# Performance work log

Hardware: AMD Instinct MI355X
Metric: run time of the kernel (lower is better)

## Reference

```python
import jax, jax.numpy as jnp
import numpy as np
import math

D_MODEL = 1024
NUM_HEADS = 16
HEAD_DIM = D_MODEL // NUM_HEADS


def _xavier(key, out_f, in_f):
    limit = math.sqrt(6.0 / (in_f + out_f))
    return jax.random.uniform(key, (out_f, in_f), jnp.float32, -limit, limit)


def ternarize(w):
    # abs-mean threshold -> {-1, 0, +1}
    abs_mean = jnp.mean(jnp.abs(w))
    return jnp.where(jnp.abs(w) > abs_mean, jnp.sign(w), jnp.zeros_like(w))


def setup_inputs() -> dict:
    key = jax.random.key(0)
    kq, kk, kv, kwq, kwk, kwv, kwo = jax.random.split(key, 7)
    B, S = 2, 2048
    return {
        "query": jax.random.normal(kq, (B, S, D_MODEL), jnp.float32),
        "key": jax.random.normal(kk, (B, S, D_MODEL), jnp.float32),
        "value": jax.random.normal(kv, (B, S, D_MODEL), jnp.float32),
        "w_q": _xavier(kwq, D_MODEL, D_MODEL),
        "w_k": _xavier(kwk, D_MODEL, D_MODEL),
        "w_v": _xavier(kwv, D_MODEL, D_MODEL),
        "w_o": _xavier(kwo, D_MODEL, D_MODEL),
    }


def reference(query, key, value, w_q, w_k, w_v, w_o):
    B, S, _ = query.shape
    # ternary projections (F.linear: x @ W.T)
    q = query @ ternarize(w_q).T
    k = key @ ternarize(w_k).T
    v = value @ ternarize(w_v).T
    # [B, H, S, Dh]
    q = q.reshape(B, S, NUM_HEADS, HEAD_DIM).transpose(0, 2, 1, 3)
    k = k.reshape(B, -1, NUM_HEADS, HEAD_DIM).transpose(0, 2, 1, 3)
    v = v.reshape(B, -1, NUM_HEADS, HEAD_DIM).transpose(0, 2, 1, 3)
    scores = jnp.einsum("bhqd,bhkd->bhqk", q, k) / math.sqrt(HEAD_DIM)
    probs = jax.nn.softmax(scores, axis=-1)
    out = jnp.einsum("bhqk,bhkd->bhqd", probs, v)
    out = out.transpose(0, 2, 1, 3).reshape(B, S, D_MODEL)
    return out @ ternarize(w_o).T
```

## Files before the change

### kernel.cpp

```cpp
#include <hip/hip_runtime.h>
#include <cstdint>
#include <cstddef>

typedef __bf16 bfloat;
typedef __bf16 bf16x8 __attribute__((ext_vector_type(8)));
typedef __bf16 bf16x4 __attribute__((ext_vector_type(4)));
typedef float  f32x4  __attribute__((ext_vector_type(4)));

static constexpr int D  = 1024;
static constexpr int S  = 2048;
static constexpr int B  = 2;
static constexpr int H  = 16;
static constexpr int DH = 64;
static constexpr int M  = B * S;
static constexpr int WMAT_N = 1024 * 1024;

#define MFMA_BF16(a, b, c) __builtin_amdgcn_mfma_f32_16x16x32_bf16((a), (b), (c), 0, 0, 0)

__device__ __forceinline__ void gl_lds16(const void* g, void* l) {
  __builtin_amdgcn_global_load_lds(
      (const __attribute__((address_space(1))) void*)g,
      (__attribute__((address_space(3))) void*)l, 16, 0, 0);
}

__global__ void prep_kernel(const float* __restrict__ w0, const float* __restrict__ w1,
                            const float* __restrict__ w2, const float* __restrict__ w3,
                            const float* __restrict__ qx, const float* __restrict__ kx,
                            const float* __restrict__ vx, bfloat* __restrict__ qhi,
                            bfloat* __restrict__ qlo, bfloat* __restrict__ khi,
                            bfloat* __restrict__ klo, bfloat* __restrict__ vhi,
                            double* __restrict__ sums) {
  const int y = blockIdx.y;
  if (y < 4) {
    const float* w = (y == 0) ? w0 : (y == 1) ? w1 : (y == 2) ? w2 : w3;
    const float4* w4 = (const float4*)w;
    double s = 0.0;
    for (int i = blockIdx.x * blockDim.x + threadIdx.x; i < (WMAT_N / 4);
         i += gridDim.x * blockDim.x) {
      float4 v = w4[i];
      s += (double)fabsf(v.x) + (double)fabsf(v.y) + (double)fabsf(v.z) + (double)fabsf(v.w);
    }
    for (int off = 1; off < 64; off <<= 1) s += __shfl_xor(s, off, 64);
    __shared__ double ps[4];
    if ((threadIdx.x & 63) == 0) ps[threadIdx.x >> 6] = s;
    __syncthreads();
    if (threadIdx.x == 0) atomicAdd(&sums[y], ps[0] + ps[1] + ps[2] + ps[3]);
  } else {
    const int z = y - 4;
    const float* x = (z == 0) ? qx : (z == 1) ? kx : vx;
    bfloat* hi = (z == 0) ? qhi : (z == 1) ? khi : vhi;
    bfloat* lo = (z == 0) ? qlo : (z == 1) ? klo : nullptr;
    const int n8 = M * D / 8;
    const float4* x4 = (const float4*)x;
    for (int i = blockIdx.x * blockDim.x + threadIdx.x; i < n8;
         i += gridDim.x * blockDim.x) {
      float4 a = x4[2 * i], b = x4[2 * i + 1];
      float f[8] = {a.x, a.y, a.z, a.w, b.x, b.y, b.z, b.w};
      bf16x8 h;
#pragma unroll
      for (int j = 0; j < 8; j++) h[j] = (bfloat)f[j];
      *(bf16x8*)&hi[(size_t)i * 8] = h;
      if (z < 2) {
        bf16x8 l;
#pragma unroll
        for (int j = 0; j < 8; j++) l[j] = (bfloat)(f[j] - (float)h[j]);
        *(bf16x8*)&lo[(size_t)i * 8] = l;
      }
    }
  }
}

__global__ void tern_kernel(const float* __restrict__ w0, const float* __restrict__ w1,
                            const float* __restrict__ w2, const float* __restrict__ w3,
                            bfloat* __restrict__ o0, bfloat* __restrict__ o1,
                            bfloat* __restrict__ o2, bfloat* __restrict__ o3,
                            const double* __restrict__ sums) {
  int z = blockIdx.y;
  const float* w = (z == 0) ? w0 : (z == 1) ? w1 : (z == 2) ? w2 : w3;
  bfloat* o = (z == 0) ? o0 : (z == 1) ? o1 : (z == 2) ? o2 : o3;
  double thr = sums[z] * (1.0 / (double)WMAT_N);
  const float4* w4 = (const float4*)w;
  for (int i = blockIdx.x * blockDim.x + threadIdx.x; i < (WMAT_N / 4);
       i += gridDim.x * blockDim.x) {
    float4 v = w4[i];
    bf16x4 r;
    r[0] = (bfloat)(((double)fabsf(v.x) > thr) ? (v.x > 0.f ? 1.f : -1.f) : 0.f);
    r[1] = (bfloat)(((double)fabsf(v.y) > thr) ? (v.y > 0.f ? 1.f : -1.f) : 0.f);
    r[2] = (bfloat)(((double)fabsf(v.z) > thr) ? (v.z > 0.f ? 1.f : -1.f) : 0.f);
    r[3] = (bfloat)(((double)fabsf(v.w) > thr) ? (v.w > 0.f ? 1.f : -1.f) : 0.f);
    *(bf16x4*)&o[(size_t)i * 4] = r;
  }
}

__global__ __launch_bounds__(256) void qkv_gemm(
    const bfloat* __restrict__ xqh, const bfloat* __restrict__ xql,
    const bfloat* __restrict__ xkh, const bfloat* __restrict__ xkl,
    const bfloat* __restrict__ xvh, const bfloat* __restrict__ wqt,
    const bfloat* __restrict__ wkt, const bfloat* __restrict__ wvt,
    bfloat* __restrict__ qmh, bfloat* __restrict__ qml,
    bfloat* __restrict__ kmh, bfloat* __restrict__ kml, bfloat* __restrict__ vtr) {
  constexpr int K = D;
  constexpr int N = D;
  __shared__ __align__(16) bfloat As0[128 * 64];
  __shared__ __align__(16) bfloat As1[128 * 64];
  __shared__ __align__(16) bfloat Ws[128 * 64];

  const int z = blockIdx.z;
  const bfloat *A0, *A1 = nullptr, *Wm;
  bfloat *Oh = nullptr, *Ol = nullptr;
  float scale = 1.f;
  bool split;
  if (z == 0) {
    A0 = xqh; A1 = xql; Wm = wqt; Oh = qmh; Ol = qml;
    scale = 0.18033688f;
    split = true;
  } else if (z == 1) {
    A0 = xkh; A1 = xkl; Wm = wkt; Oh = kmh; Ol = kml; split = true;
  } else {
    A0 = xvh; Wm = wvt; split = false;
  }

  const int t = threadIdx.x;
  const int w = t >> 6, lane = t & 63;
  const int quad = lane >> 4, l16 = lane & 15;
  const int wm = w >> 1, wn = w & 1;
  const int m0 = blockIdx.y * 128, n0 = blockIdx.x * 128;

  f32x4 acc[4][4] = {};

  const int srr = lane >> 3;
  const int spc = lane & 7;

  for (int kk = 0; kk < K; kk += 64) {
#pragma unroll
    for (int g = 0; g < 4; g++) {
      int row = w * 32 + g * 8 + srr;
      int cl = spc ^ (row & 7);
      int lo = (w * 32 + g * 8) * 64;
      gl_lds16(A0 + (size_t)(m0 + row) * K + kk + cl * 8, As0 + lo);
      if (split) gl_lds16(A1 + (size_t)(m0 + row) * K + kk + cl * 8, As1 + lo);
      gl_lds16(Wm + (size_t)(n0 + row) * K + kk + cl * 8, Ws + lo);
    }
    __syncthreads();

#pragma unroll
    for (int kidx = 0; kidx < 2; kidx++) {
      bf16x8 bfrag[4], afrag[4];
#pragma unroll
      for (int nt = 0; nt < 4; nt++) {
        int r = wn * 64 + nt * 16 + l16;
        bfrag[nt] = *(const bf16x8*)&Ws[r * 64 + (((kidx * 4 + quad) ^ (r & 7)) * 8)];
      }
#pragma unroll
      for (int mt = 0; mt < 4; mt++) {
        int r = wm * 64 + mt * 16 + l16;
        afrag[mt] = *(const bf16x8*)&As0[r * 64 + (((kidx * 4 + quad) ^ (r & 7)) * 8)];
      }
#pragma unroll
      for (int mt = 0; mt < 4; mt++)
#pragma unroll
        for (int nt = 0; nt < 4; nt++)
          acc[mt][nt] = MFMA_BF16(afrag[mt], bfrag[nt], acc[mt][nt]);
      if (split) {
#pragma unroll
        for (int mt = 0; mt < 4; mt++) {
          int r = wm * 64 + mt * 16 + l16;
          afrag[mt] = *(const bf16x8*)&As1[r * 64 + (((kidx * 4 + quad) ^ (r & 7)) * 8)];
        }
#pragma unroll
        for (int mt = 0; mt < 4; mt++)
#pragma unroll
          for (int nt = 0; nt < 4; nt++)
            acc[mt][nt] = MFMA_BF16(afrag[mt], bfrag[nt], acc[mt][nt]);
      }
    }
    __syncthreads();
  }

#pragma unroll
  for (int mt = 0; mt < 4; mt++) {
#pragma unroll
    for (int nt = 0; nt < 4; nt++) {
      const int row = m0 + wm * 64 + mt * 16 + quad * 4;
      const int col = n0 + wn * 64 + nt * 16 + l16;
      if (split) {
#pragma unroll
        for (int rg = 0; rg < 4; rg++) {
          float vv = acc[mt][nt][rg] * scale;
          size_t idx = (size_t)(row + rg) * N + col;
          bfloat hh = (bfloat)vv;
          Oh[idx] = hh;
          Ol[idx] = (bfloat)(vv - (float)hh);
        }
      } else {
        int bb = row >> 11, s = row & (S - 1);
        int kk6 = s & 63;
        int pos = (kk6 & 3) | (((kk6 >> 4) & 1) << 2) | (((kk6 >> 2) & 3) << 3) |
                  ((kk6 >> 5) << 5);
        int sp = (s & ~63) | pos;
        bf16x4 pk;
#pragma unroll
        for (int rg = 0; rg < 4; rg++) pk[rg] = (bfloat)acc[mt][nt][rg];
        *(bf16x4*)&vtr[(size_t)bb * D * S + (size_t)col * S + sp] = pk;
      }
    }
  }
}

__global__ __launch_bounds__(256, 4) void gemm_wo(const bfloat* __restrict__ A,
                                                  const bfloat* __restrict__ Wm,
                                                  float* __restrict__ Cf) {
  constexpr int K = D;
  constexpr int N = D;
  __shared__ __align__(16) bfloat As[64 * 64];
  __shared__ __align__(16) bfloat Ws[64 * 64];

  const int t = threadIdx.x;
  const int w = t >> 6, lane = t & 63;
  const int quad = lane >> 4, l16 = lane & 15;
  const int wm = w >> 1, wn = w & 1;
  const int m0 = blockIdx.y * 64, n0 = blockIdx.x * 64;

  f32x4 acc[2][2] = {};

  const int srr = lane >> 3;
  const int spc = lane & 7;

  for (int kk = 0; kk < K; kk += 64) {
#pragma unroll
    for (int g = 0; g < 2; g++) {
      int row = w * 16 + g * 8 + srr;
      int cl = spc ^ (row & 7);
      int lo = (w * 16 + g * 8) * 64;
      gl_lds16(A + (size_t)(m0 + row) * K + kk + cl * 8, As + lo);
      gl_lds16(Wm + (size_t)(n0 + row) * K + kk + cl * 8, Ws + lo);
    }
    __syncthreads();

#pragma unroll
    for (int kidx = 0; kidx < 2; kidx++) {
      bf16x8 af[2], bfr[2];
#pragma unroll
      for (int i = 0; i < 2; i++) {
        int ar = wm * 32 + i * 16 + l16;
        af[i] = *(const bf16x8*)&As[ar * 64 + (((kidx * 4 + quad) ^ (ar & 7)) * 8)];
        int br = wn * 32 + i * 16 + l16;
        bfr[i] = *(const bf16x8*)&Ws[br * 64 + (((kidx * 4 + quad) ^ (br & 7)) * 8)];
      }
#pragma unroll
      for (int mt = 0; mt < 2; mt++)
#pragma unroll
        for (int nt = 0; nt < 2; nt++)
          acc[mt][nt] = MFMA_BF16(af[mt], bfr[nt], acc[mt][nt]);
    }
    __syncthreads();
  }

#pragma unroll
  for (int mt = 0; mt < 2; mt++) {
#pragma unroll
    for (int nt = 0; nt < 2; nt++) {
      const int row = m0 + wm * 32 + mt * 16 + quad * 4;
      const int col = n0 + wn * 32 + nt * 16 + l16;
#pragma unroll
      for (int rg = 0; rg < 4; rg++) Cf[(size_t)(row + rg) * N + col] = acc[mt][nt][rg];
    }
  }
}

__global__ __launch_bounds__(256) void flash_kernel(
    const bfloat* __restrict__ qh, const bfloat* __restrict__ ql,
    const bfloat* __restrict__ kh, const bfloat* __restrict__ kl,
    const bfloat* __restrict__ vt, bfloat* __restrict__ outp) {
  __shared__ __align__(16) bfloat SM[20480];

  const int tid = threadIdx.x;
  const int w = tid >> 6, lane = tid & 63;
  const int quad = lane >> 4, l16 = lane & 15;
  const int b = blockIdx.z, h = blockIdx.y;
  const int q0 = blockIdx.x * 64;
  const size_t base = (size_t)b * S * D + (size_t)h * DH;
  const size_t vbase = (size_t)b * D * S + (size_t)h * DH * S;

  const int ssr = lane >> 3;
  const int spc = lane & 7;
  const int c8 = (spc ^ ssr) * 8;
  const int stK = w * 16 * 64;

  const bfloat* pQh = qh + base + (size_t)(q0 + w * 16 + ssr) * D + c8;
  const bfloat* pQl = ql + base + (size_t)(q0 + w * 16 + ssr) * D + c8;
  const bfloat* pKh = kh + base + (size_t)(w * 16 + ssr) * D + c8;
  const bfloat* pKl = kl + base + (size_t)(w * 16 + ssr) * D + c8;
  const bfloat* pV = vt + vbase + (size_t)(w * 16 + ssr) * S + c8;

  bf16x8 ones;
#pragma unroll
  for (int j = 0; j < 8; j++) ones[j] = (bfloat)1.f;

  gl_lds16(pQh, SM + 8192 + stK);
  gl_lds16(pQh + 8 * D, SM + 8192 + stK + 512);
  gl_lds16(pQl, SM + 12288 + stK);
  gl_lds16(pQl + 8 * D, SM + 12288 + stK + 512);
  asm volatile("s_waitcnt vmcnt(0)" ::: "memory");
  __builtin_amdgcn_s_barrier();
  asm volatile("" ::: "memory");

  const int fo0 = l16 * 64 + ((quad ^ (l16 & 7)) * 8);
  const int fo4 = fo0 ^ 32;
  const int fq = w * 1024;

  gl_lds16(pKh, SM + 0 + stK);
  gl_lds16(pKh + 8 * D, SM + 0 + stK + 512);
  gl_lds16(pKl, SM + 4096 + stK);
  gl_lds16(pKl + 8 * D, SM + 4096 + stK + 512);
  pKh += 64 * D;
  pKl += 64 * D;

  bf16x8 qhf0 = *(const bf16x8*)&SM[8192 + fq + fo0];
  bf16x8 qhf1 = *(const bf16x8*)&SM[8192 + fq + fo4];
  bf16x8 qlf0 = *(const bf16x8*)&SM[12288 + fq + fo0];
  bf16x8 qlf1 = *(const bf16x8*)&SM[12288 + fq + fo4];
  asm volatile("s_waitcnt lgkmcnt(0) vmcnt(0)" ::: "memory");

  f32x4 Oa[4] = {};
  f32x4 La = {};
  float m_i = -3.0e38f;
  constexpr int NT = S / 64;

  for (int t = 0; t < NT; ++t) {
    __builtin_amdgcn_s_barrier();
    asm volatile("" ::: "memory");
    const int cur = (t & 1) * 8192;
    const int nxt = 8192 - cur;

    gl_lds16(pV, SM + 16384 + stK);
    gl_lds16(pV + 8 * S, SM + 16384 + stK + 512);
    pV += 64;
    if (t < NT - 1) {
      gl_lds16(pKh, SM + nxt + stK);
      gl_lds16(pKh + 8 * D, SM + nxt + stK + 512);
      gl_lds16(pKl, SM + nxt + 4096 + stK);
      gl_lds16(pKl + 8 * D, SM + nxt + 4096 + stK + 512);
      pKh += 64 * D;
      pKl += 64 * D;
    }

    f32x4 sf[4];
    __builtin_amdgcn_s_setprio(1);
#pragma unroll
    for (int mt = 0; mt < 4; mt++) {
      f32x4 a = {};
      bf16x8 bh0 = *(const bf16x8*)&SM[cur + fo0 + mt * 1024];
      bf16x8 bl0 = *(const bf16x8*)&SM[cur + 4096 + fo0 + mt * 1024];
      bf16x8 bh1 = *(const bf16x8*)&SM[cur + fo4 + mt * 1024];
      bf16x8 bl1 = *(const bf16x8*)&SM[cur + 4096 + fo4 + mt * 1024];
      a = MFMA_BF16(bh0, qhf0, a);
      a = MFMA_BF16(bl0, qhf0, a);
      a = MFMA_BF16(bh0, qlf0, a);
      a = MFMA_BF16(bh1, qhf1, a);
      a = MFMA_BF16(bl1, qhf1, a);
      a = MFMA_BF16(bh1, qlf1, a);
      sf[mt] = a;
    }
    __builtin_amdgcn_s_setprio(0);

    float t0 = fmaxf(fmaxf(sf[0][0], sf[0][1]), fmaxf(sf[0][2], sf[0][3]));
    float t1 = fmaxf(fmaxf(sf[1][0], sf[1][1]), fmaxf(sf[1][2], sf[1][3]));
    float t2 = fmaxf(fmaxf(sf[2][0], sf[2][1]), fmaxf(sf[2][2], sf[2][3]));
    float t3 = fmaxf(fmaxf(sf[3][0], sf[3][1]), fmaxf(sf[3][2], sf[3][3]));
    float mm = fmaxf(fmaxf(t0, t1), fmaxf(t2, t3));
    mm = fmaxf(mm, __shfl_xor(mm, 16, 64));
    mm = fmaxf(mm, __shfl_xor(mm, 32, 64));
    if (__ballot(mm > m_i + 8.0f)) {
      float mnew = fmaxf(m_i, mm);
      float alpha = exp2f(m_i - mnew);
      m_i = mnew;
#pragma unroll
      for (int mt = 0; mt < 4; mt++) Oa[mt] *= alpha;
      La *= alpha;
    }
#pragma unroll
    for (int mt = 0; mt < 4; mt++)
#pragma unroll
      for (int rg = 0; rg < 4; rg++) sf[mt][rg] = exp2f(sf[mt][rg] - m_i);

    if (t < NT - 1)
      asm volatile("s_waitcnt vmcnt(4)" ::: "memory");
    else
      asm volatile("s_waitcnt vmcnt(0)" ::: "memory");
    __builtin_amdgcn_s_barrier();
    asm volatile("" ::: "memory");

    __builtin_amdgcn_s_setprio(1);
#pragma unroll
    for (int kp = 0; kp < 2; kp++) {
      bf16x8 pb8;
#pragma unroll
      for (int rg = 0; rg < 4; rg++) {
        pb8[rg] = (bfloat)sf[2 * kp][rg];
        pb8[4 + rg] = (bfloat)sf[2 * kp + 1][rg];
      }
      La = MFMA_BF16(ones, pb8, La);
      const int fv = kp ? fo4 : fo0;
#pragma unroll
      for (int mt = 0; mt < 4; mt++) {
        bf16x8 va = *(const bf16x8*)&SM[16384 + fv + mt * 1024];
        Oa[mt] = MFMA_BF16(va, pb8, Oa[mt]);
      }
    }
    __builtin_amdgcn_s_setprio(0);
    asm volatile("s_waitcnt vmcnt(0)" ::: "memory");
  }

  float inv = 1.0f / La[0];
  const int qrow = q0 + w * 16 + l16;
#pragma unroll
  for (int mt = 0; mt < 4; mt++) {
    bf16x4 ov;
#pragma unroll
    for (int rg = 0; rg < 4; rg++) ov[rg] = (bfloat)(Oa[mt][rg] * inv);
    *(bf16x4*)&outp[base + (size_t)qrow * D + mt * 16 + quad * 4] = ov;
  }
}

extern "C" void kernel_launch(void* const* d_in, const int* in_sizes, int n_in,
                              void* d_out, int out_size, void* d_ws, size_t ws_size,
                              hipStream_t stream) {
  const float* q_in = (const float*)d_in[0];
  const float* k_in = (const float*)d_in[1];
  const float* v_in = (const float*)d_in[2];
  const float* wq = (const float*)d_in[3];
  const float* wk = (const float*)d_in[4];
  const float* wv = (const float*)d_in[5];
  const float* wo = (const float*)d_in[6];
  float* outp = (float*)d_out;
  char* ws = (char*)d_ws;

  constexpr size_t WBYTES = (size_t)WMAT_N * 2;
  constexpr size_t XBYTES = (size_t)M * D * 2;
  size_t off = 0;
  double* sums = (double*)(ws + off); off += 256;
  bfloat* wqt = (bfloat*)(ws + off); off += WBYTES;
  bfloat* wkt = (bfloat*)(ws + off); off += WBYTES;
  bfloat* wvt = (bfloat*)(ws + off); off += WBYTES;
  bfloat* wot = (bfloat*)(ws + off); off += WBYTES;
  bfloat* xqh = (bfloat*)(ws + off); off += XBYTES;
  bfloat* xql = (bfloat*)(ws + off); off += XBYTES;
  bfloat* xkh = (bfloat*)(ws + off); off += XBYTES;
  bfloat* xkl = (bfloat*)(ws + off); off += XBYTES;
  bfloat* xvh = (bfloat*)(ws + off); off += XBYTES;
  bfloat* qmh = (bfloat*)(ws + off); off += XBYTES;
  bfloat* qml = (bfloat*)(ws + off); off += XBYTES;
  bfloat* kmh = (bfloat*)(ws + off); off += XBYTES;
  bfloat* kml = (bfloat*)(ws + off); off += XBYTES;
  bfloat* vtr = (bfloat*)(ws + off); off += XBYTES;
  bfloat* attn = xqh;

  hipMemsetAsync(sums, 0, 4 * sizeof(double), stream);
  prep_kernel<<<dim3(256, 7), 256, 0, stream>>>(
      wq, wk, wv, wo, q_in, k_in, v_in, xqh, xql, xkh, xkl, xvh, sums);
  tern_kernel<<<dim3(128, 4), 256, 0, stream>>>(wq, wk, wv, wo, wqt, wkt, wvt, wot, sums);
  qkv_gemm<<<dim3(D / 128, M / 128, 3), 256, 0, stream>>>(
      xqh, xql, xkh, xkl, xvh, wqt, wkt, wvt, qmh, qml, kmh, kml, vtr);
  flash_kernel<<<dim3(S / 64, H, B), 256, 0, stream>>>(qmh, qml, kmh, kml, vtr, attn);
  gemm_wo<<<dim3(D / 64, M / 64), 256, 0, stream>>>(attn, wot, outp);
}
```

Baseline: 300.8 us.

## Use 8-wave flash blocks over 128 queries with XCD-aware block mapping

```diff
diff --git a/kernel.cpp b/kernel.cpp
--- a/kernel.cpp
+++ b/kernel.cpp
@@ -268,7 +268,7 @@
   }
 }
 
-__global__ __launch_bounds__(256) void flash_kernel(
+__global__ __launch_bounds__(512) void flash_kernel(
     const bfloat* __restrict__ qh, const bfloat* __restrict__ ql,
     const bfloat* __restrict__ kh, const bfloat* __restrict__ kl,
     const bfloat* __restrict__ vt, bfloat* __restrict__ outp) {
@@ -277,30 +277,37 @@
   const int tid = threadIdx.x;
   const int w = tid >> 6, lane = tid & 63;
   const int quad = lane >> 4, l16 = lane & 15;
-  const int b = blockIdx.z, h = blockIdx.y;
-  const int q0 = blockIdx.x * 64;
+
+  const int blk = blockIdx.x;
+  const int xcd = blk & 7, slot = blk >> 3;
+  const int g = xcd * 4 + (slot >> 4);
+  const int h = g & 15, b = g >> 4;
+  const int q0 = (slot & 15) * 128;
+
   const size_t base = (size_t)b * S * D + (size_t)h * DH;
   const size_t vbase = (size_t)b * D * S + (size_t)h * DH * S;
 
   const int ssr = lane >> 3;
   const int spc = lane & 7;
   const int c8 = (spc ^ ssr) * 8;
-  const int stK = w * 16 * 64;
-
-  const bfloat* pQh = qh + base + (size_t)(q0 + w * 16 + ssr) * D + c8;
-  const bfloat* pQl = ql + base + (size_t)(q0 + w * 16 + ssr) * D + c8;
-  const bfloat* pKh = kh + base + (size_t)(w * 16 + ssr) * D + c8;
-  const bfloat* pKl = kl + base + (size_t)(w * 16 + ssr) * D + c8;
-  const bfloat* pV = vt + vbase + (size_t)(w * 16 + ssr) * S + c8;
+  const int stKV = w * 8 * 64;
+
+  const bfloat* pKh = kh + base + (size_t)(w * 8 + ssr) * D + c8;
+  const bfloat* pKl = kl + base + (size_t)(w * 8 + ssr) * D + c8;
+  const bfloat* pV = vt + vbase + (size_t)(w * 8 + ssr) * S + c8;
 
   bf16x8 ones;
 #pragma unroll
   for (int j = 0; j < 8; j++) ones[j] = (bfloat)1.f;
 
-  gl_lds16(pQh, SM + 8192 + stK);
-  gl_lds16(pQh + 8 * D, SM + 8192 + stK + 512);
-  gl_lds16(pQl, SM + 12288 + stK);
-  gl_lds16(pQl + 8 * D, SM + 12288 + stK + 512);
+  {
+    const bfloat* pQh = qh + base + (size_t)(q0 + w * 16 + ssr) * D + c8;
+    const bfloat* pQl = ql + base + (size_t)(q0 + w * 16 + ssr) * D + c8;
+    gl_lds16(pQh, SM + w * 1024);
+    gl_lds16(pQh + 8 * D, SM + w * 1024 + 512);
+    gl_lds16(pQl, SM + 8192 + w * 1024);
+    gl_lds16(pQl + 8 * D, SM + 8192 + w * 1024 + 512);
+  }
   asm volatile("s_waitcnt vmcnt(0)" ::: "memory");
   __builtin_amdgcn_s_barrier();
   asm volatile("" ::: "memory");
@@ -309,18 +316,19 @@
   const int fo4 = fo0 ^ 32;
   const int fq = w * 1024;
 
-  gl_lds16(pKh, SM + 0 + stK);
-  gl_lds16(pKh + 8 * D, SM + 0 + stK + 512);
-  gl_lds16(pKl, SM + 4096 + stK);
-  gl_lds16(pKl + 8 * D, SM + 4096 + stK + 512);
+  bf16x8 qhf0 = *(const bf16x8*)&SM[fq + fo0];
+  bf16x8 qhf1 = *(const bf16x8*)&SM[fq + fo4];
+  bf16x8 qlf0 = *(const bf16x8*)&SM[8192 + fq + fo0];
+  bf16x8 qlf1 = *(const bf16x8*)&SM[8192 + fq + fo4];
+  asm volatile("s_waitcnt lgkmcnt(0)" ::: "memory");
+  __builtin_amdgcn_s_barrier();
+  asm volatile("" ::: "memory");
+
+  gl_lds16(pKh, SM + 0 + stKV);
+  gl_lds16(pKl, SM + 4096 + stKV);
   pKh += 64 * D;
   pKl += 64 * D;
-
-  bf16x8 qhf0 = *(const bf16x8*)&SM[8192 + fq + fo0];
-  bf16x8 qhf1 = *(const bf16x8*)&SM[8192 + fq + fo4];
-  bf16x8 qlf0 = *(const bf16x8*)&SM[12288 + fq + fo0];
-  bf16x8 qlf1 = *(const bf16x8*)&SM[12288 + fq + fo4];
-  asm volatile("s_waitcnt lgkmcnt(0) vmcnt(0)" ::: "memory");
+  asm volatile("s_waitcnt vmcnt(0)" ::: "memory");
 
   f32x4 Oa[4] = {};
   f32x4 La = {};
@@ -333,14 +341,11 @@
     const int cur = (t & 1) * 8192;
     const int nxt = 8192 - cur;
 
-    gl_lds16(pV, SM + 16384 + stK);
-    gl_lds16(pV + 8 * S, SM + 16384 + stK + 512);
+    gl_lds16(pV, SM + 16384 + stKV);
     pV += 64;
     if (t < NT - 1) {
-      gl_lds16(pKh, SM + nxt + stK);
-      gl_lds16(pKh + 8 * D, SM + nxt + stK + 512);
-      gl_lds16(pKl, SM + nxt + 4096 + stK);
-      gl_lds16(pKl + 8 * D, SM + nxt + 4096 + stK + 512);
+      gl_lds16(pKh, SM + nxt + stKV);
+      gl_lds16(pKl, SM + nxt + 4096 + stKV);
       pKh += 64 * D;
       pKl += 64 * D;
     }
@@ -385,7 +390,7 @@
       for (int rg = 0; rg < 4; rg++) sf[mt][rg] = exp2f(sf[mt][rg] - m_i);
 
     if (t < NT - 1)
-      asm volatile("s_waitcnt vmcnt(4)" ::: "memory");
+      asm volatile("s_waitcnt vmcnt(2)" ::: "memory");
     else
       asm volatile("s_waitcnt vmcnt(0)" ::: "memory");
     __builtin_amdgcn_s_barrier();
@@ -462,6 +467,6 @@
   tern_kernel<<<dim3(128, 4), 256, 0, stream>>>(wq, wk, wv, wo, wqt, wkt, wvt, wot, sums);
   qkv_gemm<<<dim3(D / 128, M / 128, 3), 256, 0, stream>>>(
       xqh, xql, xkh, xkl, xvh, wqt, wkt, wvt, qmh, qml, kmh, kml, vtr);
-  flash_kernel<<<dim3(S / 64, H, B), 256, 0, stream>>>(qmh, qml, kmh, kml, vtr, attn);
+  flash_kernel<<<512, 512, 0, stream>>>(qmh, qml, kmh, kml, vtr, attn);
   gemm_wo<<<dim3(D / 64, M / 64), 256, 0, stream>>>(attn, wot, outp);
 }
```

Result: faster. 279.9 us (-6.9%).
